# Optimization experiments

Measured on AMD Instinct MI355X. Metric: run time of the kernel, lower is better.

The kernel has to match this reference:

```python
import jax, jax.numpy as jnp
import numpy as np

N, D = 8192, 512
SPARSITY = 0.05  # fraction of nonzero entries in originalMatrix
EPS = 1e-12      # torch F.normalize eps


def setup_inputs() -> dict:
    key = jax.random.key(0)
    k1, k2, k3 = jax.random.split(key, 3)
    vals = jax.random.normal(k1, (N, N), dtype=jnp.float32)
    keep = jax.random.uniform(k2, (N, N)) < SPARSITY
    originalMatrix = jnp.where(keep, vals, 0.0)
    featureMatrix = jax.random.normal(k3, (N, D), dtype=jnp.float32)
    return {"originalMatrix": originalMatrix, "featureMatrix": featureMatrix}


def reference(originalMatrix, featureMatrix):
    # L2-normalize rows (torch.nn.functional.normalize, p=2, dim=1)
    norm = jnp.sqrt(jnp.sum(featureMatrix * featureMatrix, axis=1, keepdims=True))
    f = featureMatrix / jnp.maximum(norm, EPS)
    # dense cosine-similarity matrix [N, N]
    new_adj = jnp.matmul(f, f.T)
    # MSE over only the nonzero entries of originalMatrix (the Python double-loop)
    mask = originalMatrix != 0
    diff = jnp.where(mask, originalMatrix - new_adj, 0.0)
    count = jnp.sum(mask).astype(new_adj.dtype)
    return jnp.sum(diff * diff) / count
```

## Files before the change

kernel.cpp:

```cpp
#include <hip/hip_runtime.h>
#include <hip/hip_bf16.h>

#define N_DIM 8192
#define D_DIM 512
#define BM 128
#define BN 128
#define BK 64
#define NTILES 2080

typedef float f32x4 __attribute__((ext_vector_type(4)));
typedef short bf16x8 __attribute__((ext_vector_type(8)));
typedef unsigned int u32;

__global__ __launch_bounds__(256) void normalize_rows_k(
    const float* __restrict__ feat, __hip_bfloat16* __restrict__ fb)
{
    const int w    = threadIdx.x >> 6;
    const int lane = threadIdx.x & 63;
    const int row  = blockIdx.x * 4 + w;

    const float* src = feat + (size_t)row * D_DIM + lane * 8;
    float4 v0 = *reinterpret_cast<const float4*>(src);
    float4 v1 = *reinterpret_cast<const float4*>(src + 4);

    float ss = v0.x*v0.x + v0.y*v0.y + v0.z*v0.z + v0.w*v0.w
             + v1.x*v1.x + v1.y*v1.y + v1.z*v1.z + v1.w*v1.w;
    #pragma unroll
    for (int off = 32; off; off >>= 1) ss += __shfl_xor(ss, off);

    const float r = 1.0f / fmaxf(sqrtf(ss), 1e-12f);

    union { ushort u[8]; uint4 q; } pk;
    float vals[8] = { v0.x, v0.y, v0.z, v0.w, v1.x, v1.y, v1.z, v1.w };
    #pragma unroll
    for (int i = 0; i < 8; ++i) {
        __hip_bfloat16 b = __float2bfloat16(vals[i] * r);
        pk.u[i] = *reinterpret_cast<ushort*>(&b);
    }
    *reinterpret_cast<uint4*>(fb + (size_t)row * D_DIM + lane * 8) = pk.q;
}

__global__ __launch_bounds__(256, 3) void fused_gemm_loss_k(
    const __hip_bfloat16* __restrict__ fb,
    const float* __restrict__ orig,
    float* __restrict__ partials)
{
    __shared__ __align__(16) __hip_bfloat16 As[BM * BK];
    __shared__ __align__(16) __hip_bfloat16 Bs[BN * BK];
    __shared__ float red[8];

    int b = blockIdx.x, br = 0;
    while (b >= 64 - br) { b -= 64 - br; ++br; }
    const int bc  = br + b;
    const int tr0 = br * BM;
    const int tc0 = bc * BN;

    const int tid  = threadIdx.x;
    const int w    = tid >> 6;
    const int lane = tid & 63;
    const int wr   = w >> 1;
    const int wc   = w & 1;
    const int fr   = lane & 15;
    const int rsub = (lane >> 4) * 4;

    f32x4 acc[4][4] = {};

    const int srow  = lane >> 3;
    const int scols = (((lane & 7) ^ (lane >> 3)) * 8);

    for (int k0 = 0; k0 < D_DIM; k0 += BK) {
        #pragma unroll
        for (int t = 0; t < 4; ++t) {
            const int c = w * 4 + t;
            const int rowA = tr0 + c * 8 + srow;
            const int rowB = tc0 + c * 8 + srow;
            const __hip_bfloat16* gA = fb + (size_t)rowA * D_DIM + k0 + scols;
            const __hip_bfloat16* gB = fb + (size_t)rowB * D_DIM + k0 + scols;
            __builtin_amdgcn_global_load_lds(
                (const __attribute__((address_space(1))) u32*)gA,
                (__attribute__((address_space(3))) u32*)(As + c * 512),
                16, 0, 0);
            __builtin_amdgcn_global_load_lds(
                (const __attribute__((address_space(1))) u32*)gB,
                (__attribute__((address_space(3))) u32*)(Bs + c * 512),
                16, 0, 0);
        }
        __syncthreads();

        const int krow = lane >> 4;
        const int sw   = (fr & 7) << 4;
        #pragma unroll
        for (int kk = 0; kk < BK; kk += 32) {
            bf16x8 af[4], bfr[4];
            #pragma unroll
            for (int fm = 0; fm < 4; ++fm) {
                const int r = wr * 64 + fm * 16 + fr;
                af[fm] = *reinterpret_cast<const bf16x8*>(
                    (const char*)As + r * 128 + (((kk << 1) + (krow << 4)) ^ sw));
            }
            #pragma unroll
            for (int fn = 0; fn < 4; ++fn) {
                const int r = wc * 64 + fn * 16 + fr;
                bfr[fn] = *reinterpret_cast<const bf16x8*>(
                    (const char*)Bs + r * 128 + (((kk << 1) + (krow << 4)) ^ sw));
            }
            #pragma unroll
            for (int fm = 0; fm < 4; ++fm)
                #pragma unroll
                for (int fn = 0; fn < 4; ++fn)
                    acc[fm][fn] = __builtin_amdgcn_mfma_f32_16x16x32_bf16(
                        af[fm], bfr[fn], acc[fm][fn], 0, 0, 0);
        }
        __syncthreads();
    }

    float lsum = 0.0f, lcnt = 0.0f;

    #pragma unroll
    for (int fm = 0; fm < 4; ++fm) {
        #pragma unroll
        for (int v = 0; v < 4; ++v) {
            const int row = tr0 + wr * 64 + fm * 16 + rsub + v;
            const float* orow = orig + (size_t)row * N_DIM + tc0 + wc * 64;
            #pragma unroll
            for (int fn = 0; fn < 4; ++fn) {
                const float o = orow[fn * 16 + fr];
                if (o != 0.0f) {
                    const float d = o - acc[fm][fn][v];
                    lsum += d * d;
                    lcnt += 1.0f;
                }
            }
        }
    }

    if (br != bc) {
        #pragma unroll
        for (int fm = 0; fm < 4; ++fm) {
            const int rbase = tr0 + wr * 64 + fm * 16 + rsub;
            #pragma unroll
            for (int fn = 0; fn < 4; ++fn) {
                const int col = tc0 + wc * 64 + fn * 16 + fr;
                const float4 o4 = *reinterpret_cast<const float4*>(
                    orig + (size_t)col * N_DIM + rbase);
                const float ov[4] = { o4.x, o4.y, o4.z, o4.w };
                #pragma unroll
                for (int v = 0; v < 4; ++v) {
                    if (ov[v] != 0.0f) {
                        const float d = ov[v] - acc[fm][fn][v];
                        lsum += d * d;
                        lcnt += 1.0f;
                    }
                }
            }
        }
    }

    #pragma unroll
    for (int off = 32; off; off >>= 1) {
        lsum += __shfl_xor(lsum, off);
        lcnt += __shfl_xor(lcnt, off);
    }
    if (lane == 0) { red[w * 2] = lsum; red[w * 2 + 1] = lcnt; }
    __syncthreads();
    if (tid == 0) {
        float s = 0.0f, c = 0.0f;
        #pragma unroll
        for (int i = 0; i < 4; ++i) { s += red[i * 2]; c += red[i * 2 + 1]; }
        partials[(size_t)blockIdx.x * 2]     = s;
        partials[(size_t)blockIdx.x * 2 + 1] = c;
    }
}

__global__ __launch_bounds__(256) void final_reduce_k(
    const float* __restrict__ partials, float* __restrict__ out, int nb)
{
    __shared__ float rs[4], rc[4];
    float s = 0.0f, c = 0.0f;
    for (int i = threadIdx.x; i < nb; i += 256) {
        s += partials[(size_t)i * 2];
        c += partials[(size_t)i * 2 + 1];
    }
    #pragma unroll
    for (int off = 32; off; off >>= 1) {
        s += __shfl_xor(s, off);
        c += __shfl_xor(c, off);
    }
    const int w = threadIdx.x >> 6, lane = threadIdx.x & 63;
    if (lane == 0) { rs[w] = s; rc[w] = c; }
    __syncthreads();
    if (threadIdx.x == 0) {
        const float S = rs[0] + rs[1] + rs[2] + rs[3];
        const float C = rc[0] + rc[1] + rc[2] + rc[3];
        out[0] = S / C;
    }
}

extern "C" void kernel_launch(void* const* d_in, const int* in_sizes, int n_in,
                              void* d_out, int out_size, void* d_ws, size_t ws_size,
                              hipStream_t stream)
{
    const float* orig = (const float*)d_in[0];
    const float* feat = (const float*)d_in[1];
    float* out = (float*)d_out;

    __hip_bfloat16* fb = (__hip_bfloat16*)d_ws;
    float* partials = (float*)((char*)d_ws + (size_t)N_DIM * D_DIM * 2);

    normalize_rows_k<<<N_DIM / 4, 256, 0, stream>>>(feat, fb);
    fused_gemm_loss_k<<<NTILES, 256, 0, stream>>>(fb, orig, partials);
    final_reduce_k<<<1, 256, 0, stream>>>(partials, out, NTILES);
}
```

Before: 88.40 us.

## Double-buffer LDS tiles with BK=32 to overlap global loads with MFMA

Replaces the single-buffered BK=64 K-loop with a double-buffered BK=32 pipeline. The next K-slice is prefetched into the alternate LDS buffer via global_load_lds while MFMAs run on the current one, with one barrier per iteration instead of two. The swizzle is reworked for the 64-byte row stride, and launch bounds rise to 4 blocks per CU. This halves per-stage LDS size but doubles iteration count and relies on manual waitcnt/barrier correctness.

```diff
diff --git a/kernel.cpp b/kernel.cpp
--- a/kernel.cpp
+++ b/kernel.cpp
@@ -5,7 +5,8 @@
 #define D_DIM 512
 #define BM 128
 #define BN 128
-#define BK 64
+#define BK 32
+#define NKT (D_DIM / BK)
 #define NTILES 2080
 
 typedef float f32x4 __attribute__((ext_vector_type(4)));
@@ -40,13 +41,13 @@
     *reinterpret_cast<uint4*>(fb + (size_t)row * D_DIM + lane * 8) = pk.q;
 }
 
-__global__ __launch_bounds__(256, 3) void fused_gemm_loss_k(
+__global__ __launch_bounds__(256, 4) void fused_gemm_loss_k(
     const __hip_bfloat16* __restrict__ fb,
     const float* __restrict__ orig,
     float* __restrict__ partials)
 {
-    __shared__ __align__(16) __hip_bfloat16 As[BM * BK];
-    __shared__ __align__(16) __hip_bfloat16 Bs[BN * BK];
+    __shared__ __align__(16) __hip_bfloat16 As[2][BM * BK];
+    __shared__ __align__(16) __hip_bfloat16 Bs[2][BN * BK];
     __shared__ float red[8];
 
     int b = blockIdx.x, br = 0;
@@ -62,56 +63,63 @@
     const int wc   = w & 1;
     const int fr   = lane & 15;
     const int rsub = (lane >> 4) * 4;
+    const int krow = lane >> 4;
 
     f32x4 acc[4][4] = {};
 
-    const int srow  = lane >> 3;
-    const int scols = (((lane & 7) ^ (lane >> 3)) * 8);
-
-    for (int k0 = 0; k0 < D_DIM; k0 += BK) {
-        #pragma unroll
-        for (int t = 0; t < 4; ++t) {
-            const int c = w * 4 + t;
-            const int rowA = tr0 + c * 8 + srow;
-            const int rowB = tc0 + c * 8 + srow;
-            const __hip_bfloat16* gA = fb + (size_t)rowA * D_DIM + k0 + scols;
-            const __hip_bfloat16* gB = fb + (size_t)rowB * D_DIM + k0 + scols;
+    auto stageAB = [&](int k0, int half) {
+        #pragma unroll
+        for (int t = 0; t < 2; ++t) {
+            const int p = (w * 2 + t) * 64 + lane;
+            const int r = p >> 2;
+            const int g = (p & 3) ^ ((r >> 1) & 3);
+            const int ko = k0 + g * 8;
+            const __hip_bfloat16* gA = fb + (size_t)(tr0 + r) * D_DIM + ko;
+            const __hip_bfloat16* gB = fb + (size_t)(tc0 + r) * D_DIM + ko;
             __builtin_amdgcn_global_load_lds(
                 (const __attribute__((address_space(1))) u32*)gA,
-                (__attribute__((address_space(3))) u32*)(As + c * 512),
+                (__attribute__((address_space(3))) u32*)(&As[half][0] + (w * 2 + t) * 512),
                 16, 0, 0);
             __builtin_amdgcn_global_load_lds(
                 (const __attribute__((address_space(1))) u32*)gB,
-                (__attribute__((address_space(3))) u32*)(Bs + c * 512),
+                (__attribute__((address_space(3))) u32*)(&Bs[half][0] + (w * 2 + t) * 512),
                 16, 0, 0);
         }
-        __syncthreads();
-
-        const int krow = lane >> 4;
-        const int sw   = (fr & 7) << 4;
-        #pragma unroll
-        for (int kk = 0; kk < BK; kk += 32) {
-            bf16x8 af[4], bfr[4];
+    };
+
+    stageAB(0, 0);
+    asm volatile("s_waitcnt vmcnt(0)" ::: "memory");
+    __builtin_amdgcn_s_barrier();
+
+    #pragma unroll
+    for (int kt = 0; kt < NKT; ++kt) {
+        const int cur = kt & 1;
+        if (kt + 1 < NKT) stageAB((kt + 1) * BK, cur ^ 1);
+
+        bf16x8 af[4], bfr[4];
+        #pragma unroll
+        for (int fm = 0; fm < 4; ++fm) {
+            const int R = wr * 64 + fm * 16 + fr;
+            af[fm] = *reinterpret_cast<const bf16x8*>(
+                (const char*)&As[cur][0] + R * 64 + ((krow ^ ((R >> 1) & 3)) << 4));
+        }
+        #pragma unroll
+        for (int fn = 0; fn < 4; ++fn) {
+            const int R = wc * 64 + fn * 16 + fr;
+            bfr[fn] = *reinterpret_cast<const bf16x8*>(
+                (const char*)&Bs[cur][0] + R * 64 + ((krow ^ ((R >> 1) & 3)) << 4));
+        }
+        #pragma unroll
+        for (int fm = 0; fm < 4; ++fm)
             #pragma unroll
-            for (int fm = 0; fm < 4; ++fm) {
-                const int r = wr * 64 + fm * 16 + fr;
-                af[fm] = *reinterpret_cast<const bf16x8*>(
-                    (const char*)As + r * 128 + (((kk << 1) + (krow << 4)) ^ sw));
-            }
-            #pragma unroll
-            for (int fn = 0; fn < 4; ++fn) {
-                const int r = wc * 64 + fn * 16 + fr;
-                bfr[fn] = *reinterpret_cast<const bf16x8*>(
-                    (const char*)Bs + r * 128 + (((kk << 1) + (krow << 4)) ^ sw));
-            }
-            #pragma unroll
-            for (int fm = 0; fm < 4; ++fm)
-                #pragma unroll
-                for (int fn = 0; fn < 4; ++fn)
-                    acc[fm][fn] = __builtin_amdgcn_mfma_f32_16x16x32_bf16(
-                        af[fm], bfr[fn], acc[fm][fn], 0, 0, 0);
-        }
-        __syncthreads();
+            for (int fn = 0; fn < 4; ++fn)
+                acc[fm][fn] = __builtin_amdgcn_mfma_f32_16x16x32_bf16(
+                    af[fm], bfr[fn], acc[fm][fn], 0, 0, 0);
+
+        if (kt + 1 < NKT) {
+            asm volatile("s_waitcnt vmcnt(0) lgkmcnt(0)" ::: "memory");
+            __builtin_amdgcn_s_barrier();
+        }
     }
 
     float lsum = 0.0f, lcnt = 0.0f;
```

After: 113.1 us. +27.9%, slower.
